# Kernel optimization log

Measured on AMD Instinct MI355X. Metric: run time of the kernel, lower is better.

Reference implementation:

```python
import jax, jax.numpy as jnp
import numpy as np

# Criterion hyperparameters (from init_kwargs)
WEIGHT_START = 1.0
WEIGHT_MAX = 5000.0
START_RAMPUP_ITERATION = 50000
N_RAMPUP_ITERATIONS = 100000
EPS = 0.001

N_CLOTH = 16384
N_OBS_VERTS = 8192
N_OBS_FACES = 16384


def setup_inputs() -> dict:
    key = jax.random.key(0)
    k1, k2, k3, k4, k5 = jax.random.split(key, 5)
    return {
        "obstacle_pos": jax.random.normal(k1, (N_OBS_VERTS, 3), dtype=jnp.float32),
        "obstacle_prev_pos": jax.random.normal(k2, (N_OBS_VERTS, 3), dtype=jnp.float32),
        "obstacle_faces": jax.random.randint(k3, (N_OBS_FACES, 3), 0, N_OBS_VERTS, dtype=jnp.int64),
        "cloth_prev_pos": jax.random.normal(k4, (N_CLOTH, 3), dtype=jnp.float32),
        "cloth_pred_pos": jax.random.normal(k5, (N_CLOTH, 3), dtype=jnp.float32),
        "iteration": 75000,
    }


def _get_weight(iteration: int) -> float:
    it = max(iteration - START_RAMPUP_ITERATION, 0)
    progress = min(it / N_RAMPUP_ITERATIONS, 1.0)
    return WEIGHT_START + (WEIGHT_MAX - WEIGHT_START) * progress


def _face_normals(pos, faces):
    # pos: [V,3], faces: [F,3] -> unit normals [F,3]
    tri = pos[faces]                      # [F,3,3]
    n = jnp.cross(tri[:, 1] - tri[:, 0], tri[:, 2] - tri[:, 0])
    return n / jnp.maximum(jnp.linalg.norm(n, axis=-1, keepdims=True), 1e-12)


def reference(obstacle_pos, obstacle_prev_pos, obstacle_faces, cloth_prev_pos, cloth_pred_pos, iteration):
    weight = _get_weight(iteration)

    tri_pos = obstacle_pos[obstacle_faces]            # [F,3,3]
    tri_prev = obstacle_prev_pos[obstacle_faces]      # [F,3,3]
    face_pos = tri_pos.mean(axis=-2)                  # [F,3] current face centers
    face_prev = tri_prev.mean(axis=-2)                # [F,3] previous face centers
    face_n = _face_normals(obstacle_pos, obstacle_faces)  # [F,3]

    # 1-NN of each cloth vertex (prev pos) among previous face centers.
    # squared distances [N,F] via ||a||^2 - 2 a.b + ||b||^2
    d2 = (
        jnp.sum(cloth_prev_pos * cloth_prev_pos, axis=-1)[:, None]
        - 2.0 * jnp.einsum("nd,fd->nf", cloth_prev_pos, face_prev)
        + jnp.sum(face_prev * face_prev, axis=-1)[None, :]
    )
    nn_idx = jnp.argmin(d2, axis=1)                   # [N]

    nn_points = face_pos[nn_idx]                      # [N,3]
    nn_normals = face_n[nn_idx]                       # [N,3]

    distance = jnp.sum((cloth_pred_pos - nn_points) * nn_normals, axis=-1)  # [N]
    interpenetration = jnp.maximum(EPS - distance, 0.0) ** 3
    # B = 1 example -> loss = sum / B * weight
    loss = interpenetration.sum() * weight
    return loss
```

## Files before the change

kernel.cpp:

```cpp
#include <hip/hip_runtime.h>
#include <hip/hip_bf16.h>
#include <stdint.h>

#define N_CLOTH     16384
#define N_OBS_VERTS 8192
#define N_OBS_FACES 16384

#define CHUNK 128
#define NC    (N_OBS_FACES / CHUNK)
#define VPT   8
#define TB    256
#define VBLK  (N_CLOTH / (TB * VPT))

__global__ __launch_bounds__(256) void k_faces(
    const float* __restrict__ obs_prev, const int* __restrict__ faces,
    float4* __restrict__ faceA, float* __restrict__ out)
{
    int f = blockIdx.x * blockDim.x + threadIdx.x;
    if (f == 0) out[0] = 0.0f;
    if (f >= N_OBS_FACES) return;
    int i0 = faces[3 * f + 0];
    int i1 = faces[3 * f + 1];
    int i2 = faces[3 * f + 2];
    float ax = obs_prev[3 * i0 + 0], ay = obs_prev[3 * i0 + 1], az = obs_prev[3 * i0 + 2];
    float bx = obs_prev[3 * i1 + 0], by = obs_prev[3 * i1 + 1], bz = obs_prev[3 * i1 + 2];
    float cx = obs_prev[3 * i2 + 0], cy = obs_prev[3 * i2 + 1], cz = obs_prev[3 * i2 + 2];
    float pcx = (ax + bx + cx) * (1.0f / 3.0f);
    float pcy = (ay + by + cy) * (1.0f / 3.0f);
    float pcz = (az + bz + cz) * (1.0f / 3.0f);
    float b2h = 0.5f * (pcx * pcx + pcy * pcy + pcz * pcz);
    faceA[f] = make_float4(pcx, pcy, pcz, b2h);
}

__global__ __launch_bounds__(TB) void k_nn(
    const float* __restrict__ cloth_prev,
    const float4* __restrict__ faceA,
    float* __restrict__ chunkMin)
{
    __shared__ float4 tile[CHUNK];
    const int t = threadIdx.x;
    const int bv = blockIdx.x;
    const int c  = blockIdx.y;
    const int fbase = c * CHUNK;

    if (t < CHUNK) tile[t] = faceA[fbase + t];

    float vx[VPT], vy[VPT], vz[VPT], best[VPT];
#pragma unroll
    for (int j = 0; j < VPT; ++j) {
        int n = bv * (TB * VPT) + j * TB + t;
        vx[j] = cloth_prev[3 * n + 0];
        vy[j] = cloth_prev[3 * n + 1];
        vz[j] = cloth_prev[3 * n + 2];
        best[j] = 3.4e38f;
    }
    __syncthreads();

#pragma unroll 2
    for (int gi = 0; gi < CHUNK / 4; ++gi) {
        float4 b0 = tile[4 * gi + 0];
        float4 b1 = tile[4 * gi + 1];
        float4 b2 = tile[4 * gi + 2];
        float4 b3 = tile[4 * gi + 3];
#pragma unroll
        for (int j = 0; j < VPT; ++j) {
            float s0 = fmaf(-vx[j], b0.x, b0.w);
            s0 = fmaf(-vy[j], b0.y, s0);
            s0 = fmaf(-vz[j], b0.z, s0);
            float s1 = fmaf(-vx[j], b1.x, b1.w);
            s1 = fmaf(-vy[j], b1.y, s1);
            s1 = fmaf(-vz[j], b1.z, s1);
            float s2 = fmaf(-vx[j], b2.x, b2.w);
            s2 = fmaf(-vy[j], b2.y, s2);
            s2 = fmaf(-vz[j], b2.z, s2);
            float s3 = fmaf(-vx[j], b3.x, b3.w);
            s3 = fmaf(-vy[j], b3.y, s3);
            s3 = fmaf(-vz[j], b3.z, s3);
            float m = fminf(fminf(s0, s1), s2);
            best[j] = fminf(fminf(m, s3), best[j]);
        }
    }

#pragma unroll
    for (int j = 0; j < VPT; ++j) {
        int n = bv * (TB * VPT) + j * TB + t;
        chunkMin[(size_t)c * N_CLOTH + n] = best[j];
    }
}

__global__ __launch_bounds__(256) void k_reduce(
    const float* __restrict__ cloth_prev,
    const float* __restrict__ cloth_pred,
    const float4* __restrict__ faceA,
    const float* __restrict__ chunkMin,
    const float* __restrict__ obs_pos,
    const int* __restrict__ faces,
    const int* __restrict__ iteration,
    float* __restrict__ out)
{
    const int t = threadIdx.x;
    const int r = t & 3;
    const int n = blockIdx.x * 64 + (t >> 2);

    float vals[NC / 4];
    float m = 3.4e38f;
#pragma unroll
    for (int i = 0; i < NC / 4; ++i) {
        vals[i] = chunkMin[(size_t)(r * (NC / 4) + i) * N_CLOTH + n];
        m = fminf(vals[i], m);
    }
    m = fminf(m, __shfl_xor(m, 1));
    m = fminf(m, __shfl_xor(m, 2));

    int cbr = 0x7FFFFFFF;
#pragma unroll
    for (int i = NC / 4 - 1; i >= 0; --i)
        cbr = (vals[i] == m) ? r * (NC / 4) + i : cbr;
    {
        int o = __shfl_xor(cbr, 1); cbr = min(cbr, o);
        o = __shfl_xor(cbr, 2); cbr = min(cbr, o);
    }
    const int cb = cbr;

    const float vx = cloth_prev[3 * n + 0];
    const float vy = cloth_prev[3 * n + 1];
    const float vz = cloth_prev[3 * n + 2];
    const int fbase = cb * CHUNK;
    int match = 0x7FFFFFFF;
#pragma unroll 8
    for (int qq = CHUNK / 4 - 1; qq >= 0; --qq) {
        int q = r * (CHUNK / 4) + qq;
        float4 b = faceA[fbase + q];
        float s = fmaf(-vx, b.x, b.w);
        s = fmaf(-vy, b.y, s);
        s = fmaf(-vz, b.z, s);
        match = (s == m) ? q : match;
    }
    {
        int o = __shfl_xor(match, 1); match = min(match, o);
        o = __shfl_xor(match, 2); match = min(match, o);
    }
    const int idx = fbase + match;

    float val = 0.0f;
    if (r == 0) {
        int i0 = faces[3 * idx + 0];
        int i1 = faces[3 * idx + 1];
        int i2 = faces[3 * idx + 2];
        float ux = obs_pos[3 * i0 + 0], uy = obs_pos[3 * i0 + 1], uz = obs_pos[3 * i0 + 2];
        float wx1 = obs_pos[3 * i1 + 0], wy1 = obs_pos[3 * i1 + 1], wz1 = obs_pos[3 * i1 + 2];
        float wx2 = obs_pos[3 * i2 + 0], wy2 = obs_pos[3 * i2 + 1], wz2 = obs_pos[3 * i2 + 2];

        float fpx = (ux + wx1 + wx2) * (1.0f / 3.0f);
        float fpy = (uy + wy1 + wy2) * (1.0f / 3.0f);
        float fpz = (uz + wz1 + wz2) * (1.0f / 3.0f);

        float e1x = wx1 - ux, e1y = wy1 - uy, e1z = wz1 - uz;
        float e2x = wx2 - ux, e2y = wy2 - uy, e2z = wz2 - uz;
        float nx = e1y * e2z - e1z * e2y;
        float ny = e1z * e2x - e1x * e2z;
        float nz = e1x * e2y - e1y * e2x;
        float nrm = sqrtf(nx * nx + ny * ny + nz * nz);
        float inv = 1.0f / fmaxf(nrm, 1e-12f);

        float px = cloth_pred[3 * n + 0];
        float py = cloth_pred[3 * n + 1];
        float pz = cloth_pred[3 * n + 2];
        float d = (px - fpx) * nx * inv + (py - fpy) * ny * inv + (pz - fpz) * nz * inv;
        float tt = fmaxf(1e-3f - d, 0.0f);
        val = tt * tt * tt;
    }

    __shared__ float red[256];
    red[t] = val;
    __syncthreads();
    for (int s = 128; s > 0; s >>= 1) {
        if (t < s) red[t] += red[t + s];
        __syncthreads();
    }
    if (t == 0) {
        int it = iteration[0];
        float itf = fmaxf((float)(it - 50000), 0.0f);
        float prog = fminf(itf * (1.0f / 100000.0f), 1.0f);
        float w = 1.0f + (5000.0f - 1.0f) * prog;
        atomicAdd(out, red[0] * w);
    }
}

extern "C" void kernel_launch(void* const* d_in, const int* in_sizes, int n_in,
                              void* d_out, int out_size, void* d_ws, size_t ws_size,
                              hipStream_t stream) {
    const float* obs_pos    = (const float*)d_in[0];
    const float* obs_prev   = (const float*)d_in[1];
    const int*   faces      = (const int*)d_in[2];
    const float* cloth_prev = (const float*)d_in[3];
    const float* cloth_pred = (const float*)d_in[4];
    const int*   iteration  = (const int*)d_in[5];
    float* out = (float*)d_out;

    char* ws = (char*)d_ws;
    float4* faceA    = (float4*)(ws);
    float*  chunkMin = (float*)(ws + 262144);

    k_faces<<<N_OBS_FACES / 256, 256, 0, stream>>>(obs_prev, faces, faceA, out);
    k_nn<<<dim3(VBLK, NC), TB, 0, stream>>>(cloth_prev, faceA, chunkMin);
    k_reduce<<<N_CLOTH * 4 / 256, 256, 0, stream>>>(
        cloth_prev, cloth_pred, faceA, chunkMin, obs_pos, faces, iteration, out);
}
```

Before: 43.54 us.

## Compute nearest-face distances with bf16x3 split MFMA instead of FP32 FMAs

Cloth vertices and face centroids are split into three bf16 pieces each and packed into K=32 fragments, so the distance term comes from 16x16x32 bf16 MFMA instructions with near-FP32 accuracy. The per-chunk minimum is reduced across lanes with shuffles and written as float4. The reduce kernel now picks the argmin with an encoded 64-bit key of distance and index. This trades extra prep work and workspace for matrix-core throughput, at the risk of small numeric differences between the MFMA minimum and the FP32 recomputation in the reduce kernel.

```diff
diff --git a/kernel.cpp b/kernel.cpp
--- a/kernel.cpp
+++ b/kernel.cpp
@@ -8,83 +8,146 @@
 
 #define CHUNK 128
 #define NC    (N_OBS_FACES / CHUNK)
-#define VPT   8
-#define TB    256
-#define VBLK  (N_CLOTH / (TB * VPT))
-
-__global__ __launch_bounds__(256) void k_faces(
+
+typedef short bf16x8 __attribute__((ext_vector_type(8)));
+typedef float f32x4  __attribute__((ext_vector_type(4)));
+
+__device__ __forceinline__ unsigned enc_f32(float x) {
+    unsigned u = __float_as_uint(x);
+    return (u & 0x80000000u) ? ~u : (u | 0x80000000u);
+}
+
+__device__ __forceinline__ void split3(float x, unsigned short* h) {
+    float f1 = __uint_as_float(__float_as_uint(x) & 0xFFFF0000u);
+    float r1 = x - f1;
+    float f2 = __uint_as_float(__float_as_uint(r1) & 0xFFFF0000u);
+    float r2 = r1 - f2;
+    h[0] = (unsigned short)(__float_as_uint(f1) >> 16);
+    h[1] = (unsigned short)(__float_as_uint(f2) >> 16);
+    h[2] = (unsigned short)(__float_as_uint(r2) >> 16);
+}
+
+__global__ __launch_bounds__(256) void k_prep(
     const float* __restrict__ obs_prev, const int* __restrict__ faces,
-    float4* __restrict__ faceA, float* __restrict__ out)
+    const float* __restrict__ cloth_prev,
+    float4* __restrict__ faceA,
+    unsigned short* __restrict__ Apk, unsigned short* __restrict__ Bpk,
+    float* __restrict__ out)
 {
-    int f = blockIdx.x * blockDim.x + threadIdx.x;
-    if (f == 0) out[0] = 0.0f;
-    if (f >= N_OBS_FACES) return;
-    int i0 = faces[3 * f + 0];
-    int i1 = faces[3 * f + 1];
-    int i2 = faces[3 * f + 2];
-    float ax = obs_prev[3 * i0 + 0], ay = obs_prev[3 * i0 + 1], az = obs_prev[3 * i0 + 2];
-    float bx = obs_prev[3 * i1 + 0], by = obs_prev[3 * i1 + 1], bz = obs_prev[3 * i1 + 2];
-    float cx = obs_prev[3 * i2 + 0], cy = obs_prev[3 * i2 + 1], cz = obs_prev[3 * i2 + 2];
-    float pcx = (ax + bx + cx) * (1.0f / 3.0f);
-    float pcy = (ay + by + cy) * (1.0f / 3.0f);
-    float pcz = (az + bz + cz) * (1.0f / 3.0f);
-    float b2h = 0.5f * (pcx * pcx + pcy * pcy + pcz * pcz);
-    faceA[f] = make_float4(pcx, pcy, pcz, b2h);
-}
-
-__global__ __launch_bounds__(TB) void k_nn(
-    const float* __restrict__ cloth_prev,
-    const float4* __restrict__ faceA,
+    int i = blockIdx.x * 256 + threadIdx.x;
+    if (i == 0) out[0] = 0.0f;
+
+    {
+        int i0 = faces[3 * i + 0];
+        int i1 = faces[3 * i + 1];
+        int i2 = faces[3 * i + 2];
+        float ax = obs_prev[3 * i0 + 0], ay = obs_prev[3 * i0 + 1], az = obs_prev[3 * i0 + 2];
+        float bx = obs_prev[3 * i1 + 0], by = obs_prev[3 * i1 + 1], bz = obs_prev[3 * i1 + 2];
+        float cx = obs_prev[3 * i2 + 0], cy = obs_prev[3 * i2 + 1], cz = obs_prev[3 * i2 + 2];
+        float pcx = (ax + bx + cx) * (1.0f / 3.0f);
+        float pcy = (ay + by + cy) * (1.0f / 3.0f);
+        float pcz = (az + bz + cz) * (1.0f / 3.0f);
+        float w = 0.5f * (pcx * pcx + pcy * pcy + pcz * pcz);
+        faceA[i] = make_float4(pcx, pcy, pcz, w);
+
+        unsigned short sx[3], sy[3], sz[3], sw[3];
+        split3(pcx, sx); split3(pcy, sy); split3(pcz, sz); split3(w, sw);
+        unsigned short B[32];
+#pragma unroll
+        for (int j = 0; j < 32; ++j) B[j] = 0;
+        B[0] = sx[0];  B[1] = sy[0];  B[2] = sz[0];
+        B[3] = sx[1];  B[4] = sy[1];  B[5] = sz[1];
+        B[6] = sx[0];  B[7] = sy[0];  B[8] = sz[0];
+        B[9] = sx[1];  B[10] = sy[1]; B[11] = sz[1];
+        B[12] = sx[2]; B[13] = sy[2]; B[14] = sz[2];
+        B[15] = sx[0]; B[16] = sy[0]; B[17] = sz[0];
+        B[18] = sw[0]; B[19] = sw[1]; B[20] = sw[2];
+        int4* dst = (int4*)(Bpk + (size_t)i * 32);
+        int4* src = (int4*)B;
+        dst[0] = src[0]; dst[1] = src[1]; dst[2] = src[2]; dst[3] = src[3];
+    }
+
+    {
+        float nx = -cloth_prev[3 * i + 0];
+        float ny = -cloth_prev[3 * i + 1];
+        float nz = -cloth_prev[3 * i + 2];
+        unsigned short sx[3], sy[3], sz[3];
+        split3(nx, sx); split3(ny, sy); split3(nz, sz);
+        unsigned short A[32];
+#pragma unroll
+        for (int j = 0; j < 32; ++j) A[j] = 0;
+        A[0] = sx[0];  A[1] = sy[0];  A[2] = sz[0];
+        A[3] = sx[0];  A[4] = sy[0];  A[5] = sz[0];
+        A[6] = sx[1];  A[7] = sy[1];  A[8] = sz[1];
+        A[9] = sx[1];  A[10] = sy[1]; A[11] = sz[1];
+        A[12] = sx[0]; A[13] = sy[0]; A[14] = sz[0];
+        A[15] = sx[2]; A[16] = sy[2]; A[17] = sz[2];
+        A[18] = 0x3F80; A[19] = 0x3F80; A[20] = 0x3F80;
+        int4* dst = (int4*)(Apk + (size_t)i * 32);
+        int4* src = (int4*)A;
+        dst[0] = src[0]; dst[1] = src[1]; dst[2] = src[2]; dst[3] = src[3];
+    }
+}
+
+__device__ __forceinline__ f32x4 min4(f32x4 a, f32x4 b) {
+    f32x4 r;
+    r.x = fminf(a.x, b.x); r.y = fminf(a.y, b.y);
+    r.z = fminf(a.z, b.z); r.w = fminf(a.w, b.w);
+    return r;
+}
+
+__global__ __launch_bounds__(256) void k_nn_mfma(
+    const unsigned short* __restrict__ Apk,
+    const unsigned short* __restrict__ Bpk,
     float* __restrict__ chunkMin)
 {
-    __shared__ float4 tile[CHUNK];
     const int t = threadIdx.x;
-    const int bv = blockIdx.x;
-    const int c  = blockIdx.y;
-    const int fbase = c * CHUNK;
-
-    if (t < CHUNK) tile[t] = faceA[fbase + t];
-
-    float vx[VPT], vy[VPT], vz[VPT], best[VPT];
-#pragma unroll
-    for (int j = 0; j < VPT; ++j) {
-        int n = bv * (TB * VPT) + j * TB + t;
-        vx[j] = cloth_prev[3 * n + 0];
-        vy[j] = cloth_prev[3 * n + 1];
-        vz[j] = cloth_prev[3 * n + 2];
-        best[j] = 3.4e38f;
-    }
-    __syncthreads();
-
-#pragma unroll 2
-    for (int gi = 0; gi < CHUNK / 4; ++gi) {
-        float4 b0 = tile[4 * gi + 0];
-        float4 b1 = tile[4 * gi + 1];
-        float4 b2 = tile[4 * gi + 2];
-        float4 b3 = tile[4 * gi + 3];
-#pragma unroll
-        for (int j = 0; j < VPT; ++j) {
-            float s0 = fmaf(-vx[j], b0.x, b0.w);
-            s0 = fmaf(-vy[j], b0.y, s0);
-            s0 = fmaf(-vz[j], b0.z, s0);
-            float s1 = fmaf(-vx[j], b1.x, b1.w);
-            s1 = fmaf(-vy[j], b1.y, s1);
-            s1 = fmaf(-vz[j], b1.z, s1);
-            float s2 = fmaf(-vx[j], b2.x, b2.w);
-            s2 = fmaf(-vy[j], b2.y, s2);
-            s2 = fmaf(-vz[j], b2.z, s2);
-            float s3 = fmaf(-vx[j], b3.x, b3.w);
-            s3 = fmaf(-vy[j], b3.y, s3);
-            s3 = fmaf(-vz[j], b3.z, s3);
-            float m = fminf(fminf(s0, s1), s2);
-            best[j] = fminf(fminf(m, s3), best[j]);
+    const int l = t & 63;
+    const int wv = t >> 6;
+    const int cid = blockIdx.y;
+    const int fb = cid * CHUNK;
+    const int vbase = blockIdx.x * 512 + wv * 128;
+    const int lrow = l & 15;
+    const int lkg = l >> 4;
+
+    bf16x8 bfr[8];
+#pragma unroll
+    for (int nt = 0; nt < 8; ++nt) {
+        int face = fb + nt * 16 + lrow;
+        bfr[nt] = *(const bf16x8*)(Bpk + (size_t)face * 32 + lkg * 8);
+    }
+
+    const f32x4 z = {0.0f, 0.0f, 0.0f, 0.0f};
+
+#pragma unroll
+    for (int mt = 0; mt < 8; ++mt) {
+        int vert = vbase + mt * 16 + lrow;
+        bf16x8 afr = *(const bf16x8*)(Apk + (size_t)vert * 32 + lkg * 8);
+
+        f32x4 a0 = __builtin_amdgcn_mfma_f32_16x16x32_bf16(afr, bfr[0], z, 0, 0, 0);
+        f32x4 a1 = __builtin_amdgcn_mfma_f32_16x16x32_bf16(afr, bfr[1], z, 0, 0, 0);
+        f32x4 a2 = __builtin_amdgcn_mfma_f32_16x16x32_bf16(afr, bfr[2], z, 0, 0, 0);
+        f32x4 a3 = __builtin_amdgcn_mfma_f32_16x16x32_bf16(afr, bfr[3], z, 0, 0, 0);
+        f32x4 a4 = __builtin_amdgcn_mfma_f32_16x16x32_bf16(afr, bfr[4], z, 0, 0, 0);
+        f32x4 a5 = __builtin_amdgcn_mfma_f32_16x16x32_bf16(afr, bfr[5], z, 0, 0, 0);
+        f32x4 a6 = __builtin_amdgcn_mfma_f32_16x16x32_bf16(afr, bfr[6], z, 0, 0, 0);
+        f32x4 a7 = __builtin_amdgcn_mfma_f32_16x16x32_bf16(afr, bfr[7], z, 0, 0, 0);
+
+        f32x4 m = min4(min4(min4(a0, a1), min4(a2, a3)),
+                       min4(min4(a4, a5), min4(a6, a7)));
+
+#pragma unroll
+        for (int d = 1; d < 16; d <<= 1) {
+            m.x = fminf(m.x, __shfl_xor(m.x, d));
+            m.y = fminf(m.y, __shfl_xor(m.y, d));
+            m.z = fminf(m.z, __shfl_xor(m.z, d));
+            m.w = fminf(m.w, __shfl_xor(m.w, d));
         }
-    }
-
-#pragma unroll
-    for (int j = 0; j < VPT; ++j) {
-        int n = bv * (TB * VPT) + j * TB + t;
-        chunkMin[(size_t)c * N_CLOTH + n] = best[j];
+        if (lrow == 0) {
+            int vo = vbase + mt * 16 + lkg * 4;
+            *(float4*)(chunkMin + (size_t)cid * N_CLOTH + vo) =
+                make_float4(m.x, m.y, m.z, m.w);
+        }
     }
 }
 
@@ -126,21 +189,23 @@
     const float vy = cloth_prev[3 * n + 1];
     const float vz = cloth_prev[3 * n + 2];
     const int fbase = cb * CHUNK;
-    int match = 0x7FFFFFFF;
+    unsigned long long bkey = 0xFFFFFFFFFFFFFFFFull;
 #pragma unroll 8
-    for (int qq = CHUNK / 4 - 1; qq >= 0; --qq) {
+    for (int qq = 0; qq < CHUNK / 4; ++qq) {
         int q = r * (CHUNK / 4) + qq;
         float4 b = faceA[fbase + q];
         float s = fmaf(-vx, b.x, b.w);
         s = fmaf(-vy, b.y, s);
         s = fmaf(-vz, b.z, s);
-        match = (s == m) ? q : match;
-    }
-    {
-        int o = __shfl_xor(match, 1); match = min(match, o);
-        o = __shfl_xor(match, 2); match = min(match, o);
-    }
-    const int idx = fbase + match;
+        unsigned long long k =
+            ((unsigned long long)enc_f32(s) << 32) | (unsigned)(fbase + q);
+        bkey = (k < bkey) ? k : bkey;
+    }
+    {
+        unsigned long long o = __shfl_xor(bkey, 1); bkey = (o < bkey) ? o : bkey;
+        o = __shfl_xor(bkey, 2); bkey = (o < bkey) ? o : bkey;
+    }
+    const int idx = (int)(unsigned)(bkey & 0xFFFFFFFFull);
 
     float val = 0.0f;
     if (r == 0) {
@@ -199,11 +264,14 @@
     float* out = (float*)d_out;
 
     char* ws = (char*)d_ws;
-    float4* faceA    = (float4*)(ws);
-    float*  chunkMin = (float*)(ws + 262144);
-
-    k_faces<<<N_OBS_FACES / 256, 256, 0, stream>>>(obs_prev, faces, faceA, out);
-    k_nn<<<dim3(VBLK, NC), TB, 0, stream>>>(cloth_prev, faceA, chunkMin);
+    float4*         faceA    = (float4*)(ws);
+    unsigned short* Apk      = (unsigned short*)(ws + 262144);
+    unsigned short* Bpk      = (unsigned short*)(ws + 1310720);
+    float*          chunkMin = (float*)(ws + 2359296);
+
+    k_prep<<<N_OBS_FACES / 256, 256, 0, stream>>>(
+        obs_prev, faces, cloth_prev, faceA, Apk, Bpk, out);
+    k_nn_mfma<<<dim3(N_CLOTH / 512, NC), 256, 0, stream>>>(Apk, Bpk, chunkMin);
     k_reduce<<<N_CLOTH * 4 / 256, 256, 0, stream>>>(
         cloth_prev, cloth_pred, faceA, chunkMin, obs_pos, faces, iteration, out);
 }
```

Measured after the change: 59.73 us. 37.2% more time.
